# Optimization experiments

Measured on AMD Instinct MI355X. Metric: run time of the kernel, lower is better.

Reference implementation:

```python
import jax, jax.numpy as jnp
import numpy as np

B, T = 64, 2048
HID, FAST, SLOW, VOCAB = 256, 64, 256, 64
WRITE_THRESH = 0.4
NEG = -1000000000.0


def setup_inputs() -> dict:
    key = jax.random.key(0)
    ks = jax.random.split(key, 10)
    s = 0.05  # small init so gate sigmoids are not saturated
    return {
        "seq": jax.random.randint(ks[0], (B, T), 0, VOCAB),
        "emb": jax.random.normal(ks[1], (VOCAB, HID), jnp.float32),        # encoder embedding table
        "Wg": jax.random.normal(ks[2], (HID, 1), jnp.float32) * s,         # write_gate
        "bg": jnp.zeros((1,), jnp.float32),
        "Wd": jax.random.normal(ks[3], (HID, 1), jnp.float32) * s,         # demotion_net
        "bd": jnp.zeros((1,), jnp.float32),
        "Wq": jax.random.normal(ks[4], (HID, HID), jnp.float32) * s,       # read_head.q_proj
        "bq": jnp.zeros((HID,), jnp.float32),
        "Wo": jax.random.normal(ks[5], (HID, VOCAB), jnp.float32) * s,     # read_head.out
        "bo": jnp.zeros((VOCAB,), jnp.float32),
    }


def _process_sequence(h, Wg, bg, Wd, bd):
    # h: (B, T, H). Sequential LRU tiered-memory scatter, vectorized over batch.
    Bb, Tt, H = h.shape

    def step(state, tok_h):
        fm, sm, fa, sa, fu, su = state
        ws = jax.nn.sigmoid(tok_h @ Wg + bg)[:, 0]          # (B,) write score
        act = ws >= WRITE_THRESH                            # skip rows with score < 0.4
        fa = fa + fu.astype(jnp.int32)                      # age occupied slots
        sa = sa + su.astype(jnp.int32)
        free = ~fu
        has_free = jnp.any(free, axis=1)                    # (B,)
        free_idx = jnp.argmax(free, axis=1)                 # first free fast slot
        dem = ((fm @ Wd)[..., 0] + bd[0])                   # (B, FAST) demotion scores
        dem_slot = jnp.argmin(dem, axis=1)
        fslot = jnp.where(has_free, free_idx, dem_slot)     # fast slot to write
        foh = jax.nn.one_hot(fslot, FAST, dtype=bool)
        wf = act[:, None] & foh                              # (B, FAST) fast-write mask
        # value demoted to slow (only used when fast was full)
        demoted = jnp.take_along_axis(fm, fslot[:, None, None], axis=1)[:, 0, :]
        slow_act = act & ~has_free
        sfree = ~su
        s_has_free = jnp.any(sfree, axis=1)
        ss = jnp.where(s_has_free, jnp.argmax(sfree, axis=1), jnp.argmax(sa, axis=1))
        soh = jax.nn.one_hot(ss, SLOW, dtype=bool)
        wsm = slow_act[:, None] & soh                        # (B, SLOW) slow-write mask
        sm = jnp.where(wsm[..., None], demoted[:, None, :], sm)
        sa = jnp.where(wsm, 0, sa)
        su = su | wsm
        tok = jax.lax.stop_gradient(tok_h)                   # original writes tok_h.detach()
        fm = jnp.where(wf[..., None], tok[:, None, :], fm)
        fa = jnp.where(wf, 0, fa)
        fu = fu | wf
        return (fm, sm, fa, sa, fu, su), None

    init = (
        jnp.zeros((Bb, FAST, H), h.dtype),
        jnp.zeros((Bb, SLOW, H), h.dtype),
        jnp.zeros((Bb, FAST), jnp.int32),
        jnp.zeros((Bb, SLOW), jnp.int32),
        jnp.zeros((Bb, FAST), bool),
        jnp.zeros((Bb, SLOW), bool),
    )
    hs = jnp.swapaxes(h[:, : Tt - 3], 0, 1)                  # loop runs for T-3 tokens
    (fm, sm, fa, sa, fu, su), _ = jax.lax.scan(step, init, hs)
    memory = jnp.concatenate([fm, sm], axis=1)               # (B, F+S, H)
    mask = jnp.concatenate([fu, su], axis=1).astype(h.dtype)
    slow_mask = su.astype(h.dtype)
    return memory, mask, slow_mask


def reference(seq, emb, Wg, bg, Wd, bd, Wq, bq, Wo, bo):
    h = emb[seq]                                             # encoder: (B, T, H)
    memory, mask, slow_mask = _process_sequence(h, Wg, bg, Wd, bd)
    # ReadHead
    q = h[:, -1, :] @ Wq + bq                                # (B, H)
    scores = jnp.einsum("bnh,bh->bn", memory, q)
    scores = jnp.where(mask == 0, NEG, scores)
    attn = jax.nn.softmax(scores, axis=-1)
    ctx = jnp.einsum("bn,bnh->bh", attn, memory)
    logits = ctx @ Wo + bo                                   # (B, VOCAB)
    return logits, slow_mask
```

## Files before the change

### kernel.cpp

```cpp
#include <hip/hip_runtime.h>
#include <math.h>

#define BB 64
#define TT 2048
#define HIDD 256
#define FASTN 64
#define SLOWN 256
#define VOC 64
#define TLOOP (TT - 3)
#define NEGC -1000000000.0f
#define EPAD 257
#define NEGBIG (-(1 << 20))
#define BYTEAT(U, J) ((int)(((U) >> (8 * (J))) & 0xFFu))

__global__ __launch_bounds__(512) void k_one(
    const int* __restrict__ seq, const float* __restrict__ emb,
    const float* __restrict__ Wg, const float* __restrict__ bg,
    const float* __restrict__ Wd, const float* __restrict__ bd,
    const float* __restrict__ Wq, const float* __restrict__ bq,
    const float* __restrict__ Wo, const float* __restrict__ bo,
    float* __restrict__ out) {
  const int b = blockIdx.x;
  const int tid = threadIdx.x;
  const int lane = tid & 63;
  const int wv = tid >> 6;

  __shared__ float embS[VOC * EPAD];
  __shared__ float WoS[HIDD * VOC];
  __shared__ __align__(16) unsigned char zsB[2080];
  __shared__ float qLastS[HIDD], ctxS[HIDD];
  __shared__ float pp[4][64];
  __shared__ float gp8[8][64], dp8[8][64];
  __shared__ float qp2[2][HIDD];
  __shared__ float demS[64], wS[64];
  __shared__ int prS[64], invS[64], cntTok[64];
  __shared__ int CS[8];
  __shared__ int PsS[8][64], QsS[8][64], aEndS[8][64], eSS[8][64];

  const int4 sq = ((const int4*)(seq + b * TT))[tid];
  const int lastv = seq[b * TT + TT - 1];
  const float4* emb4 = (const float4*)emb;
  for (int i = tid; i < VOC * 64; i += 512) {
    float4 e = emb4[i];
    float* d = &embS[(i >> 6) * EPAD + ((i & 63) << 2)];
    d[0] = e.x; d[1] = e.y; d[2] = e.z; d[3] = e.w;
  }
  {
    const float4* Wo4 = (const float4*)Wo;
    float4* WoS4 = (float4*)WoS;
    for (int i = tid; i < HIDD * VOC / 4; i += 512) WoS4[i] = Wo4[i];
  }
  __syncthreads();

  {
    const int v = tid & 63, kp = tid >> 6;
    const float* er = &embS[v * EPAD + kp * 32];
    const float* wg = &Wg[kp * 32];
    const float* wd = &Wd[kp * 32];
    float g = 0.f, d = 0.f;
#pragma unroll 8
    for (int k = 0; k < 32; ++k) { float e = er[k]; g += e * wg[k]; d += e * wd[k]; }
    gp8[kp][v] = g; dp8[kp][v] = d;
  }
  __syncthreads();
  if (tid < 64) {
    float g = bg[0], d = bd[0];
#pragma unroll
    for (int p = 0; p < 8; ++p) { g += gp8[p][tid]; d += dp8[p][tid]; }
    int act = (1.f / (1.f + expf(-g)) >= 0.4f) ? 1 : 0;
    demS[tid] = d;
    prS[tid] = act;
  }
  __syncthreads();
  if (tid < 64) {
    float dv = demS[tid];
    int r = 0;
    for (int u2 = 0; u2 < 64; ++u2) {
      float du = demS[u2];
      r += (du < dv || (du == dv && u2 < tid)) ? 1 : 0;
    }
    invS[r] = tid;
    prS[tid] = prS[tid] ? r : 0xFF;
  }
  __syncthreads();

  const int t0 = tid * 4;
  int tk[4] = {sq.x, sq.y, sq.z, sq.w};
  int by[4]; int c = 0;
#pragma unroll
  for (int j = 0; j < 4; ++j) {
    int r = prS[tk[j]];
    by[j] = (t0 + j < TLOOP) ? r : 0xFF;
    c += (by[j] != 0xFF) ? 1 : 0;
  }
  int incl = c;
  for (int s = 1; s < 64; s <<= 1) {
    int t = __shfl_up(incl, s);
    if (lane >= s) incl += t;
  }
  if (lane == 63) CS[wv] = incl;
  __syncthreads();

  int Ow = 0, A = 0;
#pragma unroll
  for (int w2 = 0; w2 < 8; ++w2) {
    int cw = CS[w2];
    Ow += (w2 < wv) ? cw : 0;
    A += cw;
  }
  {
    int pos = Ow + incl - c;
#pragma unroll
    for (int j = 0; j < 4; ++j)
      if (by[j] != 0xFF) zsB[pos++] = (unsigned char)by[j];
  }
  __syncthreads();

  const int fsplit = A < 64 ? A : 64;
  const int nL = A - fsplit;
  const int win = nL < 256 ? nL : 256;
  const int wstart = A - win;
  const int L = (((A + 7) >> 3) + 15) & ~15;
  const int baseW = wv * L;
  const int endW = min(baseW + L, A);

  int P = 0, Q = NEGBIG;
  for (int g = baseW; g < endW; g += 16) {
    uint4 t4 = *(const uint4*)(zsB + g);
    unsigned dsw[4] = {t4.x, t4.y, t4.z, t4.w};
    const int gHi = min(g + 16, endW);
    if (gHi == g + 16 && gHi <= fsplit) {
#pragma unroll
      for (int d = 0; d < 4; ++d)
#pragma unroll
        for (int j = 0; j < 4; ++j) {
          int x = (BYTEAT(dsw[d], j) <= lane) ? 1 : 0;
          P += x; Q += x;
        }
    } else if (gHi == g + 16 && g >= fsplit) {
#pragma unroll
      for (int d = 0; d < 4; ++d)
#pragma unroll
        for (int j = 0; j < 4; ++j) {
          int x = (BYTEAT(dsw[d], j) <= lane) ? 1 : 0;
          P += x - 1;
          Q = max(Q + x - 1, x);
        }
    } else {
#pragma unroll
      for (int d = 0; d < 4; ++d)
#pragma unroll
        for (int j = 0; j < 4; ++j) {
          int i = g + d * 4 + j;
          int x = (BYTEAT(dsw[d], j) <= lane) ? 1 : 0;
          bool vld = i < endW;
          bool fil = i < fsplit;
          int p = fil ? x : x - 1;
          int q = fil ? NEGBIG : x;
          int Pn = P + p;
          int Qn = max(Q + p, q);
          P = vld ? Pn : P;
          Q = vld ? Qn : Q;
        }
    }
  }
  PsS[wv][lane] = P;
  QsS[wv][lane] = Q;
  __syncthreads();

  int a = 0;
  for (int w2 = 0; w2 < wv; ++w2)
    a = max(a + PsS[w2][lane], QsS[w2][lane]);

  int e = 0;
  for (int g = baseW; g < endW; g += 16) {
    uint4 t4 = *(const uint4*)(zsB + g);
    unsigned dsw[4] = {t4.x, t4.y, t4.z, t4.w};
    const int gHi = min(g + 16, endW);
    const bool full = (gHi == g + 16);
    if (full && gHi <= fsplit) {
#pragma unroll
      for (int d = 0; d < 4; ++d)
#pragma unroll
        for (int j = 0; j < 4; ++j)
          a += (BYTEAT(dsw[d], j) <= lane) ? 1 : 0;
    } else if (full && g >= fsplit && gHi <= wstart) {
#pragma unroll
      for (int d = 0; d < 4; ++d)
#pragma unroll
        for (int j = 0; j < 4; ++j) {
          int xm1 = (BYTEAT(dsw[d], j) <= lane) ? 0 : -1;
          a = max(a, 1) + xm1;
        }
    } else if (full && g >= wstart) {
#pragma unroll
      for (int d = 0; d < 4; ++d)
#pragma unroll
        for (int j = 0; j < 4; ++j) {
          int xm1 = (BYTEAT(dsw[d], j) <= lane) ? 0 : -1;
          e += (a > 0) ? 1 : 0;
          a = max(a, 1) + xm1;
        }
    } else {
#pragma unroll
      for (int d = 0; d < 4; ++d)
#pragma unroll
        for (int j = 0; j < 4; ++j) {
          int i = g + d * 4 + j;
          int x = (BYTEAT(dsw[d], j) <= lane) ? 1 : 0;
          bool vld = i < endW;
          bool fil = i < fsplit;
          bool wg = vld && (i >= wstart);
          e += (wg && a > 0) ? 1 : 0;
          int af = a + x;
          int al = max(a, 1) + (x - 1);
          int an = fil ? af : al;
          a = vld ? an : a;
        }
    }
  }
  aEndS[wv][lane] = a;
  eSS[wv][lane] = e;
  __syncthreads();

  if (tid < 64) {
    int af = aEndS[7][lane];
    int et = 0;
#pragma unroll
    for (int w2 = 0; w2 < 8; ++w2) et += eSS[w2][lane];
    int ap = __shfl_up(af, 1); if (lane == 0) ap = 0;
    int ep = __shfl_up(et, 1); if (lane == 0) ep = 0;
    cntTok[invS[lane]] = (af - ap) + (et - ep);
  }

  {
    const int j = tid & 255, half = tid >> 8;
    const float* eL = &embS[lastv * EPAD + half * 128];
    const float* wq = &Wq[(half * 128) * HIDD + j];
    float acc = 0.f;
#pragma unroll 8
    for (int k = 0; k < 128; ++k) acc += eL[k] * wq[k * HIDD];
    qp2[half][j] = acc;
  }
  __syncthreads();
  if (tid < 256) qLastS[tid] = qp2[0][tid] + qp2[1][tid] + bq[tid];
  __syncthreads();

  if (tid < 256) {
    int v = tid & 63, part = tid >> 6;
    const float* er = &embS[v * EPAD + part * 64];
    const float* qr = &qLastS[part * 64];
    float s = 0.f;
#pragma unroll 8
    for (int k = 0; k < 64; ++k) s += er[k] * qr[k];
    pp[part][v] = s;
  }
  __syncthreads();
  if (tid < 64) {
    float sc = pp[0][tid] + pp[1][tid] + pp[2][tid] + pp[3][tid];
    int cc = cntTok[tid];
    float m = (cc > 0) ? sc : NEGC;
    for (int off = 32; off; off >>= 1) m = fmaxf(m, __shfl_xor(m, off));
    float w = (cc > 0) ? (float)cc * expf(sc - m) : 0.f;
    float z = w;
    for (int off = 32; off; off >>= 1) z += __shfl_xor(z, off);
    z += (float)(FASTN + SLOWN - (fsplit + win)) * expf(NEGC - m);
    wS[tid] = w / z;
  }
  __syncthreads();

  if (tid < 256) {
    float cacc = 0.f;
#pragma unroll 8
    for (int u = 0; u < 64; ++u) cacc += wS[u] * embS[u * EPAD + tid];
    ctxS[tid] = cacc;
  }
  __syncthreads();

  if (tid < 256) {
    int o = tid & 63, part = tid >> 6;
    const float* cr = &ctxS[part * 64];
    const float* wr = &WoS[part * 64 * VOC + o];
    float s = 0.f;
#pragma unroll 8
    for (int k = 0; k < 64; ++k) s += cr[k] * wr[k * VOC];
    pp[part][o] = s;
  }
  __syncthreads();
  if (tid < 64)
    out[b * VOC + tid] = pp[0][tid] + pp[1][tid] + pp[2][tid] + pp[3][tid] + bo[tid];
  if (tid < 256)
    out[BB * VOC + b * SLOWN + tid] = (tid < win) ? 1.0f : 0.0f;
}

extern "C" void kernel_launch(void* const* d_in, const int* in_sizes, int n_in,
                              void* d_out, int out_size, void* d_ws, size_t ws_size,
                              hipStream_t stream) {
  const int*   seq = (const int*)d_in[0];
  const float* emb = (const float*)d_in[1];
  const float* Wg  = (const float*)d_in[2];
  const float* bg  = (const float*)d_in[3];
  const float* Wd  = (const float*)d_in[4];
  const float* bd  = (const float*)d_in[5];
  const float* Wq  = (const float*)d_in[6];
  const float* bq  = (const float*)d_in[7];
  const float* Wo  = (const float*)d_in[8];
  const float* bo  = (const float*)d_in[9];
  float* out = (float*)d_out;

  k_one<<<dim3(64), dim3(512), 0, stream>>>(seq, emb, Wg, bg, Wd, bd,
                                            Wq, bq, Wo, bo, out);
}
```

Before: 95.69 us.

## Widen block to 16 wavefronts and split all per-block reductions finer

Doubles the threads per block from 512 to 1024 and has each thread handle 2 tokens instead of 4. All partial dot products (gate/demotion, q projection, scores, context, output projection) are split across 16 or 4 parts. The shared-memory staging of Wo is dropped in favour of reading it directly from global memory, and two small sync phases are merged. The aim is to shorten the serial per-block chain across the 64 blocks, at the cost of more reduction steps and higher register pressure under the 1024-thread launch bound.

```diff
diff --git a/kernel.cpp b/kernel.cpp
--- a/kernel.cpp
+++ b/kernel.cpp
@@ -12,8 +12,10 @@
 #define EPAD 257
 #define NEGBIG (-(1 << 20))
 #define BYTEAT(U, J) ((int)(((U) >> (8 * (J))) & 0xFFu))
-
-__global__ __launch_bounds__(512) void k_one(
+#define NW 16
+#define NT (NW * 64)
+
+__global__ __launch_bounds__(NT) void k_one(
     const int* __restrict__ seq, const float* __restrict__ emb,
     const float* __restrict__ Wg, const float* __restrict__ bg,
     const float* __restrict__ Wd, const float* __restrict__ bd,
@@ -26,72 +28,61 @@
   const int wv = tid >> 6;
 
   __shared__ float embS[VOC * EPAD];
-  __shared__ float WoS[HIDD * VOC];
   __shared__ __align__(16) unsigned char zsB[2080];
   __shared__ float qLastS[HIDD], ctxS[HIDD];
-  __shared__ float pp[4][64];
-  __shared__ float gp8[8][64], dp8[8][64];
-  __shared__ float qp2[2][HIDD];
+  __shared__ float pp16[NW][64];
+  __shared__ float gp16[NW][64], dp16[NW][64];
+  __shared__ float qp4[4][HIDD];
   __shared__ float demS[64], wS[64];
   __shared__ int prS[64], invS[64], cntTok[64];
-  __shared__ int CS[8];
-  __shared__ int PsS[8][64], QsS[8][64], aEndS[8][64], eSS[8][64];
-
-  const int4 sq = ((const int4*)(seq + b * TT))[tid];
+  __shared__ int CS[NW];
+  __shared__ int PsS[NW][64], QsS[NW][64], aEndS[NW][64], eSS[NW][64];
+
+  const int2 sq = ((const int2*)(seq + b * TT))[tid];
   const int lastv = seq[b * TT + TT - 1];
   const float4* emb4 = (const float4*)emb;
-  for (int i = tid; i < VOC * 64; i += 512) {
+  for (int i = tid; i < VOC * 64; i += NT) {
     float4 e = emb4[i];
     float* d = &embS[(i >> 6) * EPAD + ((i & 63) << 2)];
     d[0] = e.x; d[1] = e.y; d[2] = e.z; d[3] = e.w;
   }
-  {
-    const float4* Wo4 = (const float4*)Wo;
-    float4* WoS4 = (float4*)WoS;
-    for (int i = tid; i < HIDD * VOC / 4; i += 512) WoS4[i] = Wo4[i];
-  }
   __syncthreads();
 
   {
     const int v = tid & 63, kp = tid >> 6;
-    const float* er = &embS[v * EPAD + kp * 32];
-    const float* wg = &Wg[kp * 32];
-    const float* wd = &Wd[kp * 32];
+    const float* er = &embS[v * EPAD + kp * 16];
+    const float* wg = &Wg[kp * 16];
+    const float* wd = &Wd[kp * 16];
     float g = 0.f, d = 0.f;
-#pragma unroll 8
-    for (int k = 0; k < 32; ++k) { float e = er[k]; g += e * wg[k]; d += e * wd[k]; }
-    gp8[kp][v] = g; dp8[kp][v] = d;
+#pragma unroll
+    for (int k = 0; k < 16; ++k) { float e = er[k]; g += e * wg[k]; d += e * wd[k]; }
+    gp16[kp][v] = g; dp16[kp][v] = d;
   }
   __syncthreads();
   if (tid < 64) {
     float g = bg[0], d = bd[0];
 #pragma unroll
-    for (int p = 0; p < 8; ++p) { g += gp8[p][tid]; d += dp8[p][tid]; }
+    for (int p = 0; p < NW; ++p) { g += gp16[p][tid]; d += dp16[p][tid]; }
     int act = (1.f / (1.f + expf(-g)) >= 0.4f) ? 1 : 0;
     demS[tid] = d;
-    prS[tid] = act;
-  }
-  __syncthreads();
-  if (tid < 64) {
-    float dv = demS[tid];
+    float dv = d;
     int r = 0;
     for (int u2 = 0; u2 < 64; ++u2) {
       float du = demS[u2];
       r += (du < dv || (du == dv && u2 < tid)) ? 1 : 0;
     }
     invS[r] = tid;
-    prS[tid] = prS[tid] ? r : 0xFF;
-  }
-  __syncthreads();
-
-  const int t0 = tid * 4;
-  int tk[4] = {sq.x, sq.y, sq.z, sq.w};
-  int by[4]; int c = 0;
-#pragma unroll
-  for (int j = 0; j < 4; ++j) {
-    int r = prS[tk[j]];
-    by[j] = (t0 + j < TLOOP) ? r : 0xFF;
-    c += (by[j] != 0xFF) ? 1 : 0;
+    prS[tid] = act ? r : 0xFF;
+  }
+  __syncthreads();
+
+  const int t0 = tid * 2;
+  int by0, by1, c;
+  {
+    int r0 = prS[sq.x], r1 = prS[sq.y];
+    by0 = (t0 < TLOOP) ? r0 : 0xFF;
+    by1 = (t0 + 1 < TLOOP) ? r1 : 0xFF;
+    c = ((by0 != 0xFF) ? 1 : 0) + ((by1 != 0xFF) ? 1 : 0);
   }
   int incl = c;
   for (int s = 1; s < 64; s <<= 1) {
@@ -103,16 +94,15 @@
 
   int Ow = 0, A = 0;
 #pragma unroll
-  for (int w2 = 0; w2 < 8; ++w2) {
+  for (int w2 = 0; w2 < NW; ++w2) {
     int cw = CS[w2];
     Ow += (w2 < wv) ? cw : 0;
     A += cw;
   }
   {
     int pos = Ow + incl - c;
-#pragma unroll
-    for (int j = 0; j < 4; ++j)
-      if (by[j] != 0xFF) zsB[pos++] = (unsigned char)by[j];
+    if (by0 != 0xFF) zsB[pos++] = (unsigned char)by0;
+    if (by1 != 0xFF) zsB[pos++] = (unsigned char)by1;
   }
   __syncthreads();
 
@@ -120,7 +110,7 @@
   const int nL = A - fsplit;
   const int win = nL < 256 ? nL : 256;
   const int wstart = A - win;
-  const int L = (((A + 7) >> 3) + 15) & ~15;
+  const int L = (((A + NW - 1) / NW) + 15) & ~15;
   const int baseW = wv * L;
   const int endW = min(baseW + L, A);
 
@@ -224,40 +214,43 @@
   __syncthreads();
 
   if (tid < 64) {
-    int af = aEndS[7][lane];
+    int af = aEndS[NW - 1][lane];
     int et = 0;
 #pragma unroll
-    for (int w2 = 0; w2 < 8; ++w2) et += eSS[w2][lane];
+    for (int w2 = 0; w2 < NW; ++w2) et += eSS[w2][lane];
     int ap = __shfl_up(af, 1); if (lane == 0) ap = 0;
     int ep = __shfl_up(et, 1); if (lane == 0) ep = 0;
     cntTok[invS[lane]] = (af - ap) + (et - ep);
   }
 
   {
-    const int j = tid & 255, half = tid >> 8;
-    const float* eL = &embS[lastv * EPAD + half * 128];
-    const float* wq = &Wq[(half * 128) * HIDD + j];
+    const int j = tid & 255, kq = tid >> 8;
+    const float* eL = &embS[lastv * EPAD + kq * 64];
+    const float* wq = &Wq[(kq * 64) * HIDD + j];
     float acc = 0.f;
 #pragma unroll 8
-    for (int k = 0; k < 128; ++k) acc += eL[k] * wq[k * HIDD];
-    qp2[half][j] = acc;
-  }
-  __syncthreads();
-  if (tid < 256) qLastS[tid] = qp2[0][tid] + qp2[1][tid] + bq[tid];
-  __syncthreads();
-
-  if (tid < 256) {
-    int v = tid & 63, part = tid >> 6;
-    const float* er = &embS[v * EPAD + part * 64];
-    const float* qr = &qLastS[part * 64];
+    for (int k = 0; k < 64; ++k) acc += eL[k] * wq[k * HIDD];
+    qp4[kq][j] = acc;
+  }
+  __syncthreads();
+  if (tid < 256)
+    qLastS[tid] = qp4[0][tid] + qp4[1][tid] + qp4[2][tid] + qp4[3][tid] + bq[tid];
+  __syncthreads();
+
+  {
+    const int v = tid & 63, part = tid >> 6;
+    const float* er = &embS[v * EPAD + part * 16];
+    const float* qr = &qLastS[part * 16];
     float s = 0.f;
-#pragma unroll 8
-    for (int k = 0; k < 64; ++k) s += er[k] * qr[k];
-    pp[part][v] = s;
+#pragma unroll
+    for (int k = 0; k < 16; ++k) s += er[k] * qr[k];
+    pp16[part][v] = s;
   }
   __syncthreads();
   if (tid < 64) {
-    float sc = pp[0][tid] + pp[1][tid] + pp[2][tid] + pp[3][tid];
+    float sc = 0.f;
+#pragma unroll
+    for (int p = 0; p < NW; ++p) sc += pp16[p][tid];
     int cc = cntTok[tid];
     float m = (cc > 0) ? sc : NEGC;
     for (int off = 32; off; off >>= 1) m = fmaxf(m, __shfl_xor(m, off));
@@ -269,26 +262,35 @@
   }
   __syncthreads();
 
-  if (tid < 256) {
+  {
+    const int h = tid & 255, part = tid >> 8;
     float cacc = 0.f;
-#pragma unroll 8
-    for (int u = 0; u < 64; ++u) cacc += wS[u] * embS[u * EPAD + tid];
-    ctxS[tid] = cacc;
-  }
-  __syncthreads();
-
-  if (tid < 256) {
-    int o = tid & 63, part = tid >> 6;
-    const float* cr = &ctxS[part * 64];
-    const float* wr = &WoS[part * 64 * VOC + o];
+#pragma unroll
+    for (int u = 0; u < 16; ++u)
+      cacc += wS[part * 16 + u] * embS[(part * 16 + u) * EPAD + h];
+    qp4[part][h] = cacc;
+  }
+  __syncthreads();
+  if (tid < 256)
+    ctxS[tid] = qp4[0][tid] + qp4[1][tid] + qp4[2][tid] + qp4[3][tid];
+  __syncthreads();
+
+  {
+    const int o = tid & 63, part = tid >> 6;
+    const float* cr = &ctxS[part * 16];
+    const float* wr = &Wo[(part * 16) * VOC + o];
     float s = 0.f;
-#pragma unroll 8
-    for (int k = 0; k < 64; ++k) s += cr[k] * wr[k * VOC];
-    pp[part][o] = s;
-  }
-  __syncthreads();
-  if (tid < 64)
-    out[b * VOC + tid] = pp[0][tid] + pp[1][tid] + pp[2][tid] + pp[3][tid] + bo[tid];
+#pragma unroll
+    for (int k = 0; k < 16; ++k) s += cr[k] * wr[k * VOC];
+    pp16[part][o] = s;
+  }
+  __syncthreads();
+  if (tid < 64) {
+    float s = bo[tid];
+#pragma unroll
+    for (int p = 0; p < NW; ++p) s += pp16[p][tid];
+    out[b * VOC + tid] = s;
+  }
   if (tid < 256)
     out[BB * VOC + b * SLOWN + tid] = (tid < win) ? 1.0f : 0.0f;
 }
@@ -308,6 +310,6 @@
   const float* bo  = (const float*)d_in[9];
   float* out = (float*)d_out;
 
-  k_one<<<dim3(64), dim3(512), 0, stream>>>(seq, emb, Wg, bg, Wd, bd,
-                                            Wq, bq, Wo, bo, out);
+  k_one<<<dim3(64), dim3(NT), 0, stream>>>(seq, emb, Wg, bg, Wd, bd,
+                                           Wq, bq, Wo, bo, out);
 }
```

After: 89.98 us. 6.0% less time.
